# Optimization experiments

Measured on AMD Instinct MI355X. Metric: run time of the kernel, lower is better.

The kernel has to match this reference:

```python
import jax, jax.numpy as jnp
import numpy as np
from jax import lax

EPS = 1e-12  # torch F.normalize eps
DN = ('NCHW', 'OIHW', 'NCHW')


def setup_inputs() -> dict:
    B, C, H, W, K = 16, 64, 192, 192, 3
    key = jax.random.key(0)
    k1, k2, k3 = jax.random.split(key, 3)
    x = jax.random.normal(k1, (B, C, H, W), dtype=jnp.float32)
    # Conv2d(n_feat, 2*n_feat, 3, stride=3, bias=False) weight
    w_qk = jax.random.normal(k2, (2 * C, C, 3, 3), dtype=jnp.float32) * np.float32(np.sqrt(1.0 / (C * 9)))
    # Parameter(C,C,K,K), kaiming_normal_ (fan_in=C*K*K, gain=sqrt(2)) then *0.1
    std = np.float32(np.sqrt(2.0 / (C * K * K)) * 0.1)
    weight = jax.random.normal(k3, (C, C, K, K), dtype=jnp.float32) * std
    # temperature Parameter (1,1,1); init zeros in the module, use 0.5 so the
    # dynamic-kernel branch is exercised numerically
    temperature = jnp.full((1, 1, 1), 0.5, dtype=jnp.float32)
    return {"x": x, "w_qk": w_qk, "weight": weight, "temperature": temperature}


def _l2_normalize_per_sample(t):
    # t: (B, ...) -> L2-normalize flattened per sample (torch F.normalize)
    n = jnp.sqrt(jnp.sum(t.reshape(t.shape[0], -1) ** 2, axis=-1))
    n = jnp.maximum(n, EPS).reshape((t.shape[0],) + (1,) * (t.ndim - 1))
    return t / n


def reference(x, w_qk, weight, temperature):
    B, C, H, W = x.shape
    K = weight.shape[-1]
    S = 2 * K - 1  # 5: number of spatial shifts in the cross-covariance
    P = K - 1

    # qk conv: stride-3 valid conv -> (B, 2C, H2, W2)
    qk = lax.conv_general_dilated(x, w_qk, (3, 3), 'VALID', dimension_numbers=DN)
    q, k = jnp.split(qk, 2, axis=1)
    q = _l2_normalize_per_sample(q)
    k = _l2_normalize_per_sample(k)
    H2, W2 = q.shape[2], q.shape[3]

    # cal_xtx: attn[b, co, ci, i, j] = sum_{h,w} q_pad[b, ci, i+h, j+w] * k[b, co, h, w]
    q_pad = jnp.pad(q, ((0, 0), (0, 0), (P, P), (P, P)))
    rows = []
    for i in range(S):  # fixed small 5x5 shift set
        row = []
        for j in range(S):
            sl = lax.dynamic_slice(q_pad, (0, 0, i, j), (B, C, H2, W2))
            row.append(jnp.einsum('bchw,bdhw->bdc', sl, k))  # (B, co, ci)
        rows.append(jnp.stack(row, axis=-1))
    attn = jnp.stack(rows, axis=-2)  # (B, C, C, S, S)

    # conv2d(attn.view(B*C, C, S, S), weight) valid -> (B*C, C, K, K)
    ak = lax.conv_general_dilated(attn.reshape(B * C, C, S, S), weight, (1, 1), 'VALID', dimension_numbers=DN)
    ak = ak.reshape(B, C, C, K, K).transpose(0, 2, 1, 3, 4)  # swap the two C dims

    # normalize each (C,K,K) slice per (b, c0)
    n = jnp.sqrt(jnp.sum(ak.reshape(B, C, -1) ** 2, axis=-1))
    ak = ak / jnp.maximum(n, EPS)[:, :, None, None, None]

    kern = weight[None] + ak * temperature  # (B, C, C, K, K)

    # sample-wise conv2d: groups=B trick
    out = lax.conv_general_dilated(
        x.reshape(1, B * C, H, W), kern.reshape(B * C, C, K, K), (1, 1),
        [(K // 2, K // 2)] * 2, dimension_numbers=DN, feature_group_count=B)
    return jax.nn.relu(out.reshape(B, C, H, W))
```

## Files before the change

### kernel.cpp

```cpp
#include <hip/hip_runtime.h>
#include <cstddef>

#define BB 16
#define CC_ 64
#define HH 192
#define WW 192
#define HW2 4096
#define XPH 194
#define XPW 196

typedef _Float16 f16x8 __attribute__((ext_vector_type(8)));
typedef float f32x4 __attribute__((ext_vector_type(4)));

__global__ __launch_bounds__(1024) void k_wpack(const float* __restrict__ wqk,
                                                _Float16* __restrict__ wh) {
  int e = blockIdx.x * 1024 + threadIdx.x;
  int co = e / 576, t = e % 576;
  int ci = t / 9, rs = t % 9;
  int r = rs / 3, s = rs % 3;
  int ch = ci >> 5, t32 = ci & 31;
  wh[(((r * 2 + ch) * 128 + co) * 96) + s * 32 + t32] = (_Float16)wqk[e];
}

__global__ __launch_bounds__(256) void k_xhalo(_Float16* __restrict__ xh) {
  int e = blockIdx.x * 256 + threadIdx.x;
  int b = e / 9280, i = e % 9280;
  int r, px, c;
  if (i < 3136) {
    r = (i < 1568) ? 0 : 193;
    int j = (i < 1568) ? i : i - 1568;
    px = j >> 3;
    c = j & 7;
  } else {
    int i2 = i - 3136;
    r = 1 + (i2 >> 5);
    int rem = i2 & 31;
    int sel = rem >> 3;
    px = (sel == 0) ? 0 : 192 + sel;
    c = rem & 7;
  }
  *(f16x8*)(xh + (((size_t)b * XPH + r) * XPW + px) * 64 + c * 8) =
      (f16x8)(_Float16)0;
}

__global__ __launch_bounds__(256) void k_xpack(const float* __restrict__ x,
                                               _Float16* __restrict__ xh) {
  int blk = blockIdx.x;
  int xg = blk % 3;
  int t = blk / 3;
  int y = t % 192, b = t / 192;
  int x0 = xg * 64;
  __shared__ _Float16 tl[64 * 72];
  int tid = threadIdx.x;
  int ci = tid >> 2, c4 = (tid & 3) * 16;
  const float* xp = x + ((size_t)(b * 64 + ci) * HH + y) * WW + x0 + c4;
#pragma unroll
  for (int i = 0; i < 4; ++i) {
    float4 v = *(const float4*)(xp + i * 4);
    tl[(c4 + i * 4 + 0) * 72 + ci] = (_Float16)v.x;
    tl[(c4 + i * 4 + 1) * 72 + ci] = (_Float16)v.y;
    tl[(c4 + i * 4 + 2) * 72 + ci] = (_Float16)v.z;
    tl[(c4 + i * 4 + 3) * 72 + ci] = (_Float16)v.w;
  }
  __syncthreads();
#pragma unroll
  for (int i = 0; i < 2; ++i) {
    int e = tid + 256 * i;
    int col = e >> 3, g = e & 7;
    *(f16x8*)(xh + (((size_t)b * XPH + y + 1) * XPW + x0 + 1 + col) * 64 + g * 8) =
        *(f16x8*)&tl[col * 72 + g * 8];
  }
}

__global__ __launch_bounds__(256) void k_qkconv(const _Float16* __restrict__ xh,
                                                const _Float16* __restrict__ wh,
                                                _Float16* __restrict__ qkh) {
  int blk = blockIdx.x;
  int pt = blk & 31, b = blk >> 5;
  int tid = threadIdx.x;
  int w = tid >> 6, lane = tid & 63, n16 = lane & 15, quad = lane >> 4;
  int mh = w & 1, nh = w >> 1;
  const _Float16* xb = xh + (size_t)b * (XPH * XPW * 64);

  f32x4 acc[4][4];
#pragma unroll
  for (int mt = 0; mt < 4; ++mt)
#pragma unroll
    for (int nt = 0; nt < 4; ++nt) acc[mt][nt] = (f32x4){0.f, 0.f, 0.f, 0.f};

#pragma unroll
  for (int kc = 0; kc < 6; ++kc) {
    int r = kc >> 1, ch = kc & 1;
    int irow = 6 * pt + 3 * nh + r;
    const _Float16* wp = wh + (size_t)kc * (128 * 96);
#pragma unroll
    for (int s = 0; s < 3; ++s) {
      f16x8 af[4], bf[4];
#pragma unroll
      for (int mt = 0; mt < 4; ++mt)
        af[mt] = *(const f16x8*)(wp + (mh * 64 + mt * 16 + n16) * 96 + s * 32 +
                                 quad * 8);
#pragma unroll
      for (int nt = 0; nt < 4; ++nt) {
        int col = 3 * (nt * 16 + n16) + s;
        bf[nt] = *(const f16x8*)(xb + ((size_t)(irow + 1) * XPW + col + 1) * 64 +
                                 ch * 32 + quad * 8);
      }
#pragma unroll
      for (int mt = 0; mt < 4; ++mt)
#pragma unroll
        for (int nt = 0; nt < 4; ++nt)
          acc[mt][nt] = __builtin_amdgcn_mfma_f32_16x16x32_f16(af[mt], bf[nt],
                                                               acc[mt][nt], 0, 0, 0);
    }
  }
  int py = pt * 2 + nh;
#pragma unroll
  for (int mt = 0; mt < 4; ++mt)
#pragma unroll
    for (int reg = 0; reg < 4; ++reg) {
      int co = mh * 64 + mt * 16 + quad * 4 + reg;
      _Float16* op = qkh + (size_t)(b * 128 + co) * HW2 + py * 64;
#pragma unroll
      for (int nt = 0; nt < 4; ++nt) op[nt * 16 + n16] = (_Float16)acc[mt][nt][reg];
    }
}

__global__ __launch_bounds__(256) void k_qpad(const _Float16* __restrict__ qkh,
                                              _Float16* __restrict__ qpad) {
  int blk = blockIdx.x;
  int b = blk >> 6, ci = blk & 63;
  __shared__ _Float16 qrow[4096];
  int tid = threadIdx.x;
  const _Float16* src = qkh + (size_t)(b * 128 + ci) * HW2;
#pragma unroll
  for (int i = 0; i < 2; ++i)
    ((f16x8*)qrow)[tid + 256 * i] = ((const f16x8*)src)[tid + 256 * i];
  __syncthreads();
  _Float16* dst = qpad + ((size_t)(b * 5) * 64 + ci) * 4352;
  for (int it = tid; it < 2720; it += 256) {
    int w8 = it & 7;
    int hr = (it >> 3) % 68;
    int djx = (it >> 3) / 68;
    int h = hr - 2;
    f16x8 v = (f16x8)(_Float16)0;
    if ((unsigned)h < 64u) {
#pragma unroll
      for (int j = 0; j < 8; ++j) {
        int c = w8 * 8 + j + djx - 2;
        if ((unsigned)c < 64u) v[j] = qrow[h * 64 + c];
      }
    }
    *(f16x8*)(dst + (size_t)djx * (64 * 4352) + hr * 64 + w8 * 8) = v;
  }
}

__global__ __launch_bounds__(256) void k_attn(const _Float16* __restrict__ qkh,
                                              const _Float16* __restrict__ qpad,
                                              float* __restrict__ attn_p) {
  int blk = blockIdx.x;
  int sp = blk & 1;
  int t = blk >> 1;
  int sh = t % 25, b = t / 25;
  int djx = sh % 5, dix = sh / 5;
  const _Float16* kb = qkh + (size_t)(b * 128 + 64) * HW2;
  const _Float16* qpb = qpad + ((size_t)(b * 5 + djx) * 64) * 4352 + dix * 64;
  __shared__ __align__(16) _Float16 ks[64 * 264];
  __shared__ __align__(16) _Float16 qs[64 * 264];
  int tid = threadIdx.x, w = tid >> 6, lane = tid & 63;
  int n16 = lane & 15, quad = lane >> 4;

  f32x4 acc[4][4];
#pragma unroll
  for (int mt = 0; mt < 4; ++mt)
#pragma unroll
    for (int nt = 0; nt < 4; ++nt) acc[mt][nt] = (f32x4){0.f, 0.f, 0.f, 0.f};

  for (int c = 0; c < 8; ++c) {
    int p0 = sp * 2048 + c * 256;
    __syncthreads();
#pragma unroll
    for (int i = 0; i < 8; ++i) {
      int e = tid + 256 * i;
      int g = e & 31, row = e >> 5;
      *(f16x8*)&ks[row * 264 + g * 8] =
          *(const f16x8*)(kb + (size_t)row * HW2 + p0 + g * 8);
      *(f16x8*)&qs[row * 264 + g * 8] =
          *(const f16x8*)(qpb + (size_t)row * 4352 + p0 + g * 8);
    }
    __syncthreads();
#pragma unroll
    for (int ki = 0; ki < 2; ++ki) {
      int ko = (w * 2 + ki) * 32 + quad * 8;
      f16x8 af[4], bf[4];
#pragma unroll
      for (int mt = 0; mt < 4; ++mt)
        af[mt] = *(const f16x8*)&ks[(mt * 16 + n16) * 264 + ko];
#pragma unroll
      for (int nt = 0; nt < 4; ++nt)
        bf[nt] = *(const f16x8*)&qs[(nt * 16 + n16) * 264 + ko];
#pragma unroll
      for (int mt = 0; mt < 4; ++mt)
#pragma unroll
        for (int nt = 0; nt < 4; ++nt)
          acc[mt][nt] = __builtin_amdgcn_mfma_f32_16x16x32_f16(af[mt], bf[nt],
                                                               acc[mt][nt], 0, 0, 0);
    }
  }
  float* racc = (float*)ks;
  __syncthreads();
  for (int e = tid; e < 64 * 66; e += 256) racc[e] = 0.f;
  __syncthreads();
#pragma unroll
  for (int mt = 0; mt < 4; ++mt) {
    int co = mt * 16 + quad * 4;
#pragma unroll
    for (int reg = 0; reg < 4; ++reg)
#pragma unroll
      for (int nt = 0; nt < 4; ++nt)
        atomicAdd(&racc[(co + reg) * 66 + nt * 16 + n16], acc[mt][nt][reg]);
  }
  __syncthreads();
  float* op = attn_p + (size_t)(b * 25 + sh) * 4096;
  for (int e = tid; e < 4096; e += 256)
    atomicAdd(&op[e], racc[(e >> 6) * 66 + (e & 63)]);
}

__global__ __launch_bounds__(576) void k_akconv(const float* __restrict__ attn_p,
                                                const float* __restrict__ wgt,
                                                float* __restrict__ akt) {
  int blk = blockIdx.x;
  int b = blk >> 6, co = blk & 63;
  __shared__ float sa[64 * 25];
  int tid = threadIdx.x;
  for (int e = tid; e < 1600; e += 576) {
    int didj = e >> 6, ci = e & 63;
    size_t idx = (((size_t)b * 25 + didj) * 64 + co) * 64 + ci;
    sa[ci * 25 + didj] = attn_p[idx];
  }
  __syncthreads();
  int o = tid / 9, rs = tid % 9;
  int ki = rs / 3, kj = rs % 3;
  float acc = 0.f;
  for (int ci = 0; ci < 64; ++ci) {
    const float* wp = wgt + (o * 64 + ci) * 9;
    const float* ap = sa + ci * 25 + ki * 5 + kj;
#pragma unroll
    for (int r = 0; r < 3; ++r)
#pragma unroll
      for (int s = 0; s < 3; ++s) acc += ap[r * 5 + s] * wp[r * 3 + s];
  }
  akt[((size_t)(b * 64 + o) * 64 + co) * 9 + rs] = acc;
}

__global__ __launch_bounds__(576) void k_kern(const float* __restrict__ akt,
                                              const float* __restrict__ wgt,
                                              const float* __restrict__ temp,
                                              _Float16* __restrict__ kh) {
  int blk = blockIdx.x;
  int o = blk & 63;
  int tid = threadIdx.x;
  float v = akt[(size_t)blk * 576 + tid];
  float sq = v * v;
#pragma unroll
  for (int m = 1; m < 64; m <<= 1) sq += __shfl_xor(sq, m, 64);
  __shared__ float wsum[9];
  if ((tid & 63) == 0) wsum[tid >> 6] = sq;
  __syncthreads();
  float tot = 0.f;
#pragma unroll
  for (int i = 0; i < 9; ++i) tot += wsum[i];
  float inv = temp[0] / fmaxf(sqrtf(tot), 1e-12f);
  float kv = wgt[o * 576 + tid] + v * inv;
  int b = blk >> 6;
  int ci = tid / 9, rs = tid % 9;
  kh[(((size_t)(b * 9 + rs) * 64 + o) * 64) + ci] = (_Float16)kv;
}

__global__ __launch_bounds__(256) void k_final(const _Float16* __restrict__ xh,
                                               const _Float16* __restrict__ kh,
                                               float* __restrict__ out) {
  int blk = blockIdx.x;
  int xt = blk % 3;
  int t2 = blk / 3;
  int yt = t2 % 48, b = t2 / 48;
  int y0 = yt * 4, x0 = xt * 64;

  __shared__ __align__(16) _Float16 xs[6 * 68 * 64];

  int tid = threadIdx.x;
  int w = tid >> 6, lane = tid & 63;
  int n16 = lane & 15, quad = lane >> 4;

  const _Float16* xb = xh + (size_t)b * (XPH * XPW * 64);
  const _Float16* kb = kh + (size_t)b * (9 * 64 * 64);

  {
    f16x8 v[13];
#pragma unroll
    for (int i = 0; i < 13; ++i) {
      int e = tid + 256 * i;
      if (e < 3264) {
        int row = e / 544, rem = e % 544;
        int px = rem >> 3, c = rem & 7;
        v[i] = *(const f16x8*)(xb + ((size_t)(y0 + row) * XPW + x0 + px) * 64 +
                               c * 8);
      }
    }
#pragma unroll
    for (int i = 0; i < 13; ++i) {
      int e = tid + 256 * i;
      if (e < 3264) {
        int row = e / 544, rem = e % 544;
        int px = rem >> 3, c = rem & 7;
        *(f16x8*)&xs[((row * 68 + px) * 8 + (c ^ (px & 7))) * 8] = v[i];
      }
    }
  }
  __syncthreads();

  f32x4 acc[4][4];
#pragma unroll
  for (int mt = 0; mt < 4; ++mt)
#pragma unroll
    for (int nt = 0; nt < 4; ++nt) acc[mt][nt] = (f32x4){0.f, 0.f, 0.f, 0.f};

#pragma unroll
  for (int ch = 0; ch < 18; ++ch) {
    int rs = ch >> 1, hi = ch & 1;
    int r = rs / 3, s = rs % 3;
    int trow = w + r;
    f16x8 af[4], bf[4];
#pragma unroll
    for (int mt = 0; mt < 4; ++mt)
      af[mt] = *(const f16x8*)(kb + ((size_t)rs * 64 + mt * 16 + n16) * 64 +
                               hi * 32 + quad * 8);
#pragma unroll
    for (int nt = 0; nt < 4; ++nt) {
      int px = nt * 16 + n16 + s;
      int c = (hi * 4 + quad) ^ (px & 7);
      bf[nt] = *(const f16x8*)&xs[((trow * 68 + px) * 8 + c) * 8];
    }
#pragma unroll
    for (int mt = 0; mt < 4; ++mt)
#pragma unroll
      for (int nt = 0; nt < 4; ++nt)
        acc[mt][nt] = __builtin_amdgcn_mfma_f32_16x16x32_f16(af[mt], bf[nt],
                                                             acc[mt][nt], 0, 0, 0);
  }

  int y = y0 + w;
#pragma unroll
  for (int mt = 0; mt < 4; ++mt)
#pragma unroll
    for (int reg = 0; reg < 4; ++reg) {
      int o = mt * 16 + quad * 4 + reg;
      float* op = out + (((size_t)(b * 64 + o) * HH + y) * WW + x0);
#pragma unroll
      for (int nt = 0; nt < 4; ++nt)
        op[nt * 16 + n16] = fmaxf(acc[mt][nt][reg], 0.f);
    }
}

extern "C" void kernel_launch(void* const* d_in, const int* in_sizes, int n_in,
                              void* d_out, int out_size, void* d_ws, size_t ws_size,
                              hipStream_t stream) {
  const float* x = (const float*)d_in[0];
  const float* wqk = (const float*)d_in[1];
  const float* wgt = (const float*)d_in[2];
  const float* temp = (const float*)d_in[3];
  float* out = (float*)d_out;
  char* ws = (char*)d_ws;

  _Float16* xh = (_Float16*)ws;
  _Float16* qkh = (_Float16*)(ws + 77873152);
  _Float16* qpad = (_Float16*)(ws + 94650368);
  float* attn_p = (float*)(ws + 139214848);
  _Float16* wh = (_Float16*)(ws + 139067392);
  float* akt = (float*)(ws + 94650368);
  _Float16* kh = (_Float16*)(ws + 97009664);

  hipMemsetAsync(attn_p, 0, 6553600, stream);
  k_wpack<<<dim3(72), 1024, 0, stream>>>(wqk, wh);
  k_xhalo<<<dim3(580), 256, 0, stream>>>(xh);
  k_xpack<<<dim3(9216), 256, 0, stream>>>(x, xh);
  k_qkconv<<<dim3(512), 256, 0, stream>>>(xh, wh, qkh);
  k_qpad<<<dim3(1024), 256, 0, stream>>>(qkh, qpad);
  k_attn<<<dim3(800), 256, 0, stream>>>(qkh, qpad, attn_p);
  k_akconv<<<dim3(1024), 576, 0, stream>>>(attn_p, wgt, akt);
  k_kern<<<dim3(1024), 576, 0, stream>>>(akt, wgt, temp, kh);
  k_final<<<dim3(2304), 256, 0, stream>>>(xh, kh, out);
}
```

Before: 609.0 us.

## Stream attn operands from global, vectorize qpad shifts, prefetch final weights

k_qpad now loads three adjacent 8-wide vectors once and builds all five column-shifted outputs with register shuffles, replacing per-element LDS reads. k_attn drops its LDS staging of k and q, loads MFMA fragments straight from global memory, and remaps blocks so each XCD handles particular batches for L2 locality. k_final prefetches weight fragments two steps ahead in a rotating register buffer and requests 3 blocks per SM through launch bounds. Together these aim to cut LDS traffic and barriers and to hide load latency, at the cost of uncoalesced global fragment loads and higher register pressure.

```diff
diff --git a/kernel.cpp b/kernel.cpp
--- a/kernel.cpp
+++ b/kernel.cpp
@@ -138,20 +138,25 @@
     ((f16x8*)qrow)[tid + 256 * i] = ((const f16x8*)src)[tid + 256 * i];
   __syncthreads();
   _Float16* dst = qpad + ((size_t)(b * 5) * 64 + ci) * 4352;
-  for (int it = tid; it < 2720; it += 256) {
-    int w8 = it & 7;
-    int hr = (it >> 3) % 68;
-    int djx = (it >> 3) / 68;
+  const f16x8 zero = (f16x8)(_Float16)0;
+  for (int it = tid; it < 544; it += 256) {
+    int w8 = it & 7, hr = it >> 3;
     int h = hr - 2;
-    f16x8 v = (f16x8)(_Float16)0;
-    if ((unsigned)h < 64u) {
+    bool rowok = (unsigned)h < 64u;
+    f16x8 vm = (rowok && w8 > 0) ? *(const f16x8*)&qrow[h * 64 + w8 * 8 - 8] : zero;
+    f16x8 vc = rowok ? *(const f16x8*)&qrow[h * 64 + w8 * 8] : zero;
+    f16x8 vp = (rowok && w8 < 7) ? *(const f16x8*)&qrow[h * 64 + w8 * 8 + 8] : zero;
+#pragma unroll
+    for (int djx = 0; djx < 5; ++djx) {
+      const int s = djx - 2;
+      f16x8 r;
 #pragma unroll
       for (int j = 0; j < 8; ++j) {
-        int c = w8 * 8 + j + djx - 2;
-        if ((unsigned)c < 64u) v[j] = qrow[h * 64 + c];
+        const int rel = j + s;
+        r[j] = (rel < 0) ? vm[8 + rel] : ((rel < 8) ? vc[rel] : vp[rel - 8]);
       }
-    }
-    *(f16x8*)(dst + (size_t)djx * (64 * 4352) + hr * 64 + w8 * 8) = v;
+      *(f16x8*)(dst + (size_t)djx * (64 * 4352) + hr * 64 + w8 * 8) = r;
+    }
   }
 }
 
@@ -159,58 +164,45 @@
                                               const _Float16* __restrict__ qpad,
                                               float* __restrict__ attn_p) {
   int blk = blockIdx.x;
-  int sp = blk & 1;
-  int t = blk >> 1;
-  int sh = t % 25, b = t / 25;
+  int xcd = blk & 7, j = blk >> 3;
+  int b = xcd + ((j >= 50) ? 8 : 0);
+  int t = (j >= 50) ? (j - 50) : j;
+  int sh = t >> 1, sp = t & 1;
   int djx = sh % 5, dix = sh / 5;
   const _Float16* kb = qkh + (size_t)(b * 128 + 64) * HW2;
   const _Float16* qpb = qpad + ((size_t)(b * 5 + djx) * 64) * 4352 + dix * 64;
-  __shared__ __align__(16) _Float16 ks[64 * 264];
-  __shared__ __align__(16) _Float16 qs[64 * 264];
   int tid = threadIdx.x, w = tid >> 6, lane = tid & 63;
   int n16 = lane & 15, quad = lane >> 4;
 
+  __shared__ float racc[64 * 66];
+  for (int e = tid; e < 64 * 66; e += 256) racc[e] = 0.f;
+  __syncthreads();
+
   f32x4 acc[4][4];
 #pragma unroll
   for (int mt = 0; mt < 4; ++mt)
 #pragma unroll
     for (int nt = 0; nt < 4; ++nt) acc[mt][nt] = (f32x4){0.f, 0.f, 0.f, 0.f};
 
-  for (int c = 0; c < 8; ++c) {
-    int p0 = sp * 2048 + c * 256;
-    __syncthreads();
-#pragma unroll
-    for (int i = 0; i < 8; ++i) {
-      int e = tid + 256 * i;
-      int g = e & 31, row = e >> 5;
-      *(f16x8*)&ks[row * 264 + g * 8] =
-          *(const f16x8*)(kb + (size_t)row * HW2 + p0 + g * 8);
-      *(f16x8*)&qs[row * 264 + g * 8] =
-          *(const f16x8*)(qpb + (size_t)row * 4352 + p0 + g * 8);
-    }
-    __syncthreads();
-#pragma unroll
-    for (int ki = 0; ki < 2; ++ki) {
-      int ko = (w * 2 + ki) * 32 + quad * 8;
-      f16x8 af[4], bf[4];
-#pragma unroll
-      for (int mt = 0; mt < 4; ++mt)
-        af[mt] = *(const f16x8*)&ks[(mt * 16 + n16) * 264 + ko];
+  int base = sp * 2048 + w * 512 + quad * 8;
+#pragma unroll 4
+  for (int ks = 0; ks < 16; ++ks) {
+    int p0 = base + ks * 32;
+    f16x8 af[4], bf[4];
+#pragma unroll
+    for (int mt = 0; mt < 4; ++mt)
+      af[mt] = *(const f16x8*)(kb + (size_t)(mt * 16 + n16) * HW2 + p0);
+#pragma unroll
+    for (int nt = 0; nt < 4; ++nt)
+      bf[nt] = *(const f16x8*)(qpb + (size_t)(nt * 16 + n16) * 4352 + p0);
+#pragma unroll
+    for (int mt = 0; mt < 4; ++mt)
 #pragma unroll
       for (int nt = 0; nt < 4; ++nt)
-        bf[nt] = *(const f16x8*)&qs[(nt * 16 + n16) * 264 + ko];
-#pragma unroll
-      for (int mt = 0; mt < 4; ++mt)
-#pragma unroll
-        for (int nt = 0; nt < 4; ++nt)
-          acc[mt][nt] = __builtin_amdgcn_mfma_f32_16x16x32_f16(af[mt], bf[nt],
-                                                               acc[mt][nt], 0, 0, 0);
-    }
-  }
-  float* racc = (float*)ks;
-  __syncthreads();
-  for (int e = tid; e < 64 * 66; e += 256) racc[e] = 0.f;
-  __syncthreads();
+        acc[mt][nt] = __builtin_amdgcn_mfma_f32_16x16x32_f16(af[mt], bf[nt],
+                                                             acc[mt][nt], 0, 0, 0);
+  }
+
 #pragma unroll
   for (int mt = 0; mt < 4; ++mt) {
     int co = mt * 16 + quad * 4;
@@ -277,9 +269,9 @@
   kh[(((size_t)(b * 9 + rs) * 64 + o) * 64) + ci] = (_Float16)kv;
 }
 
-__global__ __launch_bounds__(256) void k_final(const _Float16* __restrict__ xh,
-                                               const _Float16* __restrict__ kh,
-                                               float* __restrict__ out) {
+__global__ __launch_bounds__(256, 3) void k_final(const _Float16* __restrict__ xh,
+                                                  const _Float16* __restrict__ kh,
+                                                  float* __restrict__ out) {
   int blk = blockIdx.x;
   int xt = blk % 3;
   int t2 = blk / 3;
@@ -325,16 +317,25 @@
 #pragma unroll
     for (int nt = 0; nt < 4; ++nt) acc[mt][nt] = (f32x4){0.f, 0.f, 0.f, 0.f};
 
+#define LDAF(dst, ch_)                                                          \
+  {                                                                             \
+    const int rs_ = (ch_) >> 1, hi_ = (ch_)&1;                                  \
+    _Pragma("unroll") for (int mt = 0; mt < 4; ++mt) dst[mt] =                  \
+        *(const f16x8*)(kb + ((size_t)rs_ * 64 + mt * 16 + n16) * 64 +          \
+                        hi_ * 32 + quad * 8);                                   \
+  }
+
+  f16x8 af[3][4];
+  LDAF(af[0], 0)
+  LDAF(af[1], 1)
+
 #pragma unroll
   for (int ch = 0; ch < 18; ++ch) {
+    if (ch + 2 < 18) LDAF(af[(ch + 2) % 3], ch + 2)
     int rs = ch >> 1, hi = ch & 1;
     int r = rs / 3, s = rs % 3;
     int trow = w + r;
-    f16x8 af[4], bf[4];
-#pragma unroll
-    for (int mt = 0; mt < 4; ++mt)
-      af[mt] = *(const f16x8*)(kb + ((size_t)rs * 64 + mt * 16 + n16) * 64 +
-                               hi * 32 + quad * 8);
+    f16x8 bf[4];
 #pragma unroll
     for (int nt = 0; nt < 4; ++nt) {
       int px = nt * 16 + n16 + s;
@@ -345,9 +346,11 @@
     for (int mt = 0; mt < 4; ++mt)
 #pragma unroll
       for (int nt = 0; nt < 4; ++nt)
-        acc[mt][nt] = __builtin_amdgcn_mfma_f32_16x16x32_f16(af[mt], bf[nt],
-                                                             acc[mt][nt], 0, 0, 0);
-  }
+        acc[mt][nt] = __builtin_amdgcn_mfma_f32_16x16x32_f16(af[ch % 3][mt],
+                                                             bf[nt], acc[mt][nt],
+                                                             0, 0, 0);
+  }
+#undef LDAF
 
   int y = y0 + w;
 #pragma unroll
```

New measurement: 602.7 us. Within noise of the previous version (-1.0%).
